# Performance work log

Hardware: AMD Instinct MI355X
Metric: run time of the kernel (lower is better)

## Reference

```python
import jax, jax.numpy as jnp
import numpy as np

N_NODES = 20000
N_EDGES = 320000
NUM_FEATURES = 128
CUTOFF = 5.0
NUM_RBF = 20
EPS = 1e-8


def setup_inputs() -> dict:
    key = jax.random.key(0)
    ks = jax.random.split(key, 10)
    v = jax.random.normal(ks[0], (N_NODES, NUM_FEATURES, 3), dtype=jnp.float32)
    s = jax.random.normal(ks[1], (N_NODES, NUM_FEATURES), dtype=jnp.float32)
    # edge list: col0 = src idx, col1 = dst idx (js), cols 2:5 = displacement vector
    src = jax.random.randint(ks[2], (N_EDGES,), 0, N_NODES).astype(jnp.float32)
    dst = jax.random.randint(ks[3], (N_EDGES,), 0, N_NODES).astype(jnp.float32)
    vec = jax.random.normal(ks[4], (N_EDGES, 3), dtype=jnp.float32) * 2.0
    r = jnp.concatenate([src[:, None], dst[:, None], vec], axis=1)
    # s_path params (torch Linear weight [out,in] -> stored here as [in,out])
    W1 = jax.random.normal(ks[5], (NUM_FEATURES, NUM_FEATURES), dtype=jnp.float32) * np.sqrt(2.0 / NUM_FEATURES)
    b1 = jnp.zeros((NUM_FEATURES,), dtype=jnp.float32)
    W2 = jax.random.normal(ks[6], (NUM_FEATURES, 3 * NUM_FEATURES), dtype=jnp.float32) * np.sqrt(2.0 / NUM_FEATURES)
    b2 = jnp.zeros((3 * NUM_FEATURES,), dtype=jnp.float32)
    # r_path params
    Wr = jax.random.normal(ks[7], (NUM_RBF, 3 * NUM_FEATURES), dtype=jnp.float32) * np.sqrt(1.0 / NUM_RBF)
    br = jnp.zeros((3 * NUM_FEATURES,), dtype=jnp.float32)
    return {"v": v, "s": s, "r": r, "W1": W1, "b1": b1, "W2": W2, "b2": b2, "Wr": Wr, "br": br}


def reference(v, s, r, W1, b1, W2, b2, Wr, br):
    nf = NUM_FEATURES
    js = r[:, 1].astype(jnp.int32)          # [E] destination node indices
    rv = r[:, 2:]                            # [E,3] displacement vectors

    # s_path: Linear -> SiLU -> Linear, computed per-node then gathered
    h = s @ W1 + b1
    phi = (h * jax.nn.sigmoid(h)) @ W2 + b2  # [N, 3*nf]

    # RBF expansion of edge distances
    norm_r = jnp.linalg.norm(rv, axis=1, keepdims=True)          # [E,1]
    norm_c = jnp.clip(norm_r, EPS)
    n = jnp.arange(1, NUM_RBF + 1, dtype=rv.dtype)[None, :]      # [1,20]
    rbf = jnp.clip(jnp.sin(n * (jnp.pi / CUTOFF) * norm_c) / (norm_c + EPS), -1.0, 1.0)

    # r_path Linear then cosine cutoff applied elementwise to the features
    Wf = rbf @ Wr + br                                            # [E, 3*nf]
    Wf = 0.5 * (jnp.cos(jnp.pi * Wf / CUTOFF) + 1.0) * (Wf < CUTOFF).astype(Wf.dtype)

    pre = phi[js, :] * Wf                                         # [E, 3*nf]
    split_1 = pre[:, :nf]
    split_2 = pre[:, nf:2 * nf]
    split_3 = pre[:, 2 * nf:]

    # NOTE: original code divides the normalized vector by the norm again
    rvn = rv / (norm_r + EPS)
    dir_term = rvn / (norm_r + EPS)                               # [E,3]
    left_2 = v[js, :, :] * split_1[:, :, None] + split_3[:, :, None] * dir_term[:, None, :]

    delta_v = jnp.zeros_like(v).at[js].add(left_2)
    delta_s = jnp.zeros_like(s).at[js].add(split_2)
    return (delta_v, delta_s)
```

## Files before the change

kernel.cpp:

```cpp
#include <hip/hip_runtime.h>
#include <math.h>

#define NND 20000
#define NE  320000
#define NF  128
#define NRBF 20
#define DEGCAP 64

typedef float f32x4 __attribute__((ext_vector_type(4)));
typedef short bf16x8 __attribute__((ext_vector_type(8)));

static constexpr float FCUT = 5.0f;
static constexpr float FEPS = 1e-8f;

__device__ __forceinline__ unsigned short f2bf(float x) {
    unsigned int u = __builtin_bit_cast(unsigned int, x);
    u += 0x7FFFu + ((u >> 16) & 1u);
    return (unsigned short)(u >> 16);
}
__device__ __forceinline__ float bf2f(unsigned short h) {
    unsigned int u = ((unsigned int)h) << 16;
    return __builtin_bit_cast(float, u);
}

__global__ __launch_bounds__(256) void scatter2_k(const float* __restrict__ r,
                                                  int* __restrict__ cursor,
                                                  float4* __restrict__ payload) {
    int e = blockIdx.x * 256 + threadIdx.x;
    if (e >= NE) return;
    const float* re = r + (size_t)e * 5;
    int j = (int)re[1];
    float x = re[2], y = re[3], z = re[4];
    float nrm = sqrtf(x * x + y * y + z * z);
    float inv = 1.0f / ((nrm + FEPS) * (nrm + FEPS));
    int pos = atomicAdd(&cursor[j], 1);
    if (pos < DEGCAP)
        payload[((size_t)j << 6) + pos] = make_float4(x * inv, y * inv, z * inv, nrm);
}

__global__ __launch_bounds__(256) void pack_all_k(const float* __restrict__ W1,
                                                  const float* __restrict__ W2,
                                                  const float* __restrict__ Wr,
                                                  const float* __restrict__ br,
                                                  unsigned short* __restrict__ Wp1,
                                                  unsigned short* __restrict__ Wp2,
                                                  unsigned short* __restrict__ WrP) {
    int fid = blockIdx.x * 256 + threadIdx.x;
    if (fid < 2048) {
        int lane = fid & 63, kk = (fid >> 6) & 3, nch = fid >> 8;
        int col = nch * 16 + (lane & 15);
        int k0 = kk * 32 + ((lane >> 4) * 8);
        unsigned short* o = Wp1 + (size_t)fid * 8;
#pragma unroll
        for (int j = 0; j < 8; j++) o[j] = f2bf(W1[(size_t)(k0 + j) * 128 + col]);
    } else if (fid < 2048 + 6144) {
        int f2 = fid - 2048;
        int lane = f2 & 63, kk = (f2 >> 6) & 3, nch = f2 >> 8;
        int col = nch * 16 + (lane & 15);
        int k0 = kk * 32 + ((lane >> 4) * 8);
        unsigned short* o = Wp2 + (size_t)f2 * 8;
#pragma unroll
        for (int j = 0; j < 8; j++) o[j] = f2bf(W2[(size_t)(k0 + j) * 384 + col]);
    } else if (fid < 2048 + 6144 + 1536) {
        int f3 = fid - 8192;
        int lane = f3 & 63, ft = f3 >> 6;
        int col = ft * 16 + (lane & 15);
        int k0 = (lane >> 4) * 8;
        unsigned short* o = WrP + (size_t)f3 * 8;
#pragma unroll
        for (int j = 0; j < 8; j++) {
            int k = k0 + j;
            float val = (k < NRBF) ? Wr[(size_t)k * 384 + col] : ((k == NRBF) ? br[col] : 0.0f);
            o[j] = f2bf(val);
        }
    }
}

__global__ __launch_bounds__(256) void mlp_k(const float* __restrict__ s,
                                             const unsigned short* __restrict__ Wp1,
                                             const float* __restrict__ b1,
                                             const unsigned short* __restrict__ Wp2,
                                             const float* __restrict__ b2,
                                             unsigned short* __restrict__ phi) {
    __shared__ unsigned short lds[4 * 8192];
    int tid = threadIdx.x;
    int lane = tid & 63, wave = tid >> 6;
    int node0 = blockIdx.x * 64 + wave * 16;
    int arow = lane & 15, kgrp = lane >> 4;
    unsigned short* hW = lds + wave * 8192;
    unsigned short* pW = hW + 2048;

    int anode = node0 + arow; if (anode > NND - 1) anode = NND - 1;
    const float* ap = s + (size_t)anode * NF + kgrp * 8;
    bf16x8 afrag[4];
#pragma unroll
    for (int kk = 0; kk < 4; kk++) {
        float4 x0 = *(const float4*)(ap + kk * 32);
        float4 x1 = *(const float4*)(ap + kk * 32 + 4);
        union { unsigned short u[8]; bf16x8 v; } c;
        c.u[0] = f2bf(x0.x); c.u[1] = f2bf(x0.y); c.u[2] = f2bf(x0.z); c.u[3] = f2bf(x0.w);
        c.u[4] = f2bf(x1.x); c.u[5] = f2bf(x1.y); c.u[6] = f2bf(x1.z); c.u[7] = f2bf(x1.w);
        afrag[kk] = c.v;
    }
    f32x4 acc[8];
#pragma unroll
    for (int n = 0; n < 8; n++) acc[n] = (f32x4)(0.0f);
    const bf16x8* W8a = (const bf16x8*)Wp1;
#pragma unroll
    for (int nch = 0; nch < 8; nch++)
#pragma unroll
        for (int kk = 0; kk < 4; kk++)
            acc[nch] = __builtin_amdgcn_mfma_f32_16x16x32_bf16(
                afrag[kk], W8a[(nch * 4 + kk) * 64 + lane], acc[nch], 0, 0, 0);
#pragma unroll
    for (int nch = 0; nch < 8; nch++) {
        int col = nch * 16 + arow;
        float bb = b1[col];
#pragma unroll
        for (int rg = 0; rg < 4; rg++) {
            int row = kgrp * 4 + rg;
            float x = acc[nch][rg] + bb;
            float y = x / (1.0f + __expf(-x));
            hW[row * 128 + col] = f2bf(y);
        }
    }
    __syncthreads();
    bf16x8 hfrag[4];
#pragma unroll
    for (int kk = 0; kk < 4; kk++)
        hfrag[kk] = *(const bf16x8*)(hW + arow * 128 + kk * 32 + kgrp * 8);
#pragma unroll
    for (int c = 0; c < 3; c++) {
        f32x4 acc2[8];
#pragma unroll
        for (int n = 0; n < 8; n++) acc2[n] = (f32x4)(0.0f);
        const bf16x8* W8b = (const bf16x8*)Wp2;
#pragma unroll
        for (int nch = 0; nch < 8; nch++)
#pragma unroll
            for (int kk = 0; kk < 4; kk++)
                acc2[nch] = __builtin_amdgcn_mfma_f32_16x16x32_bf16(
                    hfrag[kk], W8b[((c * 8 + nch) * 4 + kk) * 64 + lane], acc2[nch], 0, 0, 0);
#pragma unroll
        for (int nch = 0; nch < 8; nch++) {
            int colg = c * 128 + nch * 16 + arow;
            float bb = b2[colg];
#pragma unroll
            for (int rg = 0; rg < 4; rg++) {
                int row = kgrp * 4 + rg;
                pW[row * 384 + colg] = f2bf(acc2[nch][rg] + bb);
            }
        }
    }
    __syncthreads();
#pragma unroll
    for (int it = 0; it < 12; it++) {
        int idx = it * 64 + lane;
        int row = idx / 48, ch = idx - row * 48;
        int node = node0 + row;
        if (node < NND) {
            uint4 val = *(const uint4*)(pW + row * 384 + ch * 8);
            *(uint4*)(phi + (size_t)node * 384 + ch * 8) = val;
        }
    }
}

__global__ __launch_bounds__(256) void reduce6_k(const int* __restrict__ cursor,
                                                 const float4* __restrict__ payload,
                                                 const unsigned short* __restrict__ phi,
                                                 const float* __restrict__ v,
                                                 const unsigned short* __restrict__ WrP,
                                                 float* __restrict__ dv,
                                                 float* __restrict__ ds) {
    int tid = threadIdx.x;
    int lane = tid & 63;
    int la = lane & 15, kg = lane >> 4;
    int gwid = blockIdx.x * 4 + (tid >> 6);
    int w = gwid & 1;
    int jstart = gwid >> 1;
    int jstride = (gridDim.x * 4) >> 1;

    bool isKg2 = (kg == 2), isKg3 = (kg == 3);

    bf16x8 wrf[12];
#pragma unroll
    for (int q = 0; q < 12; q++)
        wrf[q] = *(const bf16x8*)(WrP + (size_t)(((2 * q + w) << 6) + lane) * 8);

    for (int j = jstart; j < NND; j += jstride) {
        int deg = cursor[j]; if (deg > DEGCAP) deg = DEGCAP;
        const float4* pay = payload + ((size_t)j << 6);

        int f = (2 * kg + w) * 16 + la;
        const unsigned short* ph = phi + (size_t)j * 384;
        float p1 = bf2f(ph[f]), p2 = bf2f(ph[128 + f]), p3 = bf2f(ph[256 + f]);
        size_t vb = ((size_t)j * NF + f) * 3;
        float vx = v[vb], vy = v[vb + 1], vz = v[vb + 2];

        float a0[4], a1[4], sdx[4], sdy[4], sdz[4];
        float DX = 0.f, DY = 0.f, DZ = 0.f;
#pragma unroll
        for (int i = 0; i < 4; i++) { a0[i] = 0.f; a1[i] = 0.f; sdx[i] = 0.f; sdy[i] = 0.f; sdz[i] = 0.f; }

        for (int base = 0; base < deg; base += 16) {
            int cnt = deg - base; if (cnt > 16) cnt = 16;
            float4 p = pay[base + (la < cnt ? la : cnt - 1)];
            float nc = fmaxf(p.w, FEPS);
            float invd = 1.0f / (nc + FEPS);
            float sv[8];
#pragma unroll
            for (int j2 = 0; j2 < 8; j2++) {
                int k = kg * 8 + j2;
                float s0 = __builtin_amdgcn_sinf((float)(k + 1) * 0.1f * nc) * invd;
                sv[j2] = fminf(fmaxf(s0, -1.f), 1.f);
            }
            unsigned int w0, w1, w2, w3;
            asm("v_cvt_pk_bf16_f32 %0, %1, %2" : "=v"(w0) : "v"(sv[0]), "v"(sv[1]));
            asm("v_cvt_pk_bf16_f32 %0, %1, %2" : "=v"(w1) : "v"(sv[2]), "v"(sv[3]));
            asm("v_cvt_pk_bf16_f32 %0, %1, %2" : "=v"(w2) : "v"(sv[4]), "v"(sv[5]));
            asm("v_cvt_pk_bf16_f32 %0, %1, %2" : "=v"(w3) : "v"(sv[6]), "v"(sv[7]));
            w2 = isKg2 ? 0x00003F80u : w2;
            w0 = isKg3 ? 0u : w0;
            w1 = isKg3 ? 0u : w1;
            w2 = isKg3 ? 0u : w2;
            w3 = (kg >= 2) ? 0u : w3;
            union { unsigned int w[4]; bf16x8 v8; } af;
            af.w[0] = w0; af.w[1] = w1; af.w[2] = w2; af.w[3] = w3;
            float dx[4], dy[4], dz[4], lim[4];
#pragma unroll
            for (int rr = 0; rr < 4; rr++) {
                int er = kg * 4 + rr;
                dx[rr] = __shfl(p.x, er);
                dy[rr] = __shfl(p.y, er);
                dz[rr] = __shfl(p.z, er);
                lim[rr] = (er < cnt) ? FCUT : -3.4e38f;
            }
            DX += dx[0] + dx[1] + dx[2] + dx[3];
            DY += dy[0] + dy[1] + dy[2] + dy[3];
            DZ += dz[0] + dz[1] + dz[2] + dz[3];
#pragma unroll
            for (int q = 0; q < 12; q++) {
                f32x4 d = __builtin_amdgcn_mfma_f32_16x16x32_bf16(
                    af.v8, wrf[q], (f32x4)(0.0f), 0, 0, 0);
#pragma unroll
                for (int rr = 0; rr < 4; rr++) {
                    float a = d[rr];
                    float c = __builtin_amdgcn_cosf(a * 0.1f);
                    float t = (a < lim[rr]) ? c : -1.0f;
                    if (q < 4)      a0[q] += t;
                    else if (q < 8) a1[q - 4] += t;
                    else {
                        sdx[q - 8] = fmaf(t, dx[rr], sdx[q - 8]);
                        sdy[q - 8] = fmaf(t, dy[rr], sdy[q - 8]);
                        sdz[q - 8] = fmaf(t, dz[rr], sdz[q - 8]);
                    }
                }
            }
        }
#pragma unroll
        for (int i = 0; i < 4; i++) {
            a0[i] += __shfl_xor(a0[i], 16);  a0[i] += __shfl_xor(a0[i], 32);
            a1[i] += __shfl_xor(a1[i], 16);  a1[i] += __shfl_xor(a1[i], 32);
            sdx[i] += __shfl_xor(sdx[i], 16); sdx[i] += __shfl_xor(sdx[i], 32);
            sdy[i] += __shfl_xor(sdy[i], 16); sdy[i] += __shfl_xor(sdy[i], 32);
            sdz[i] += __shfl_xor(sdz[i], 16); sdz[i] += __shfl_xor(sdz[i], 32);
        }
        DX += __shfl_xor(DX, 16); DX += __shfl_xor(DX, 32);
        DY += __shfl_xor(DY, 16); DY += __shfl_xor(DY, 32);
        DZ += __shfl_xor(DZ, 16); DZ += __shfl_xor(DZ, 32);
        float R = (float)(((deg + 15) >> 4) << 4);

        float A0 = 0, A1 = 0, SX = 0, SY = 0, SZ = 0;
#pragma unroll
        for (int i = 0; i < 4; i++) {
            if (kg == i) { A0 = a0[i]; A1 = a1[i]; SX = sdx[i]; SY = sdy[i]; SZ = sdz[i]; }
        }
        float sum1 = 0.5f * (A0 + R);
        float sum2 = 0.5f * (A1 + R);
        float sx = 0.5f * (SX + DX);
        float sy = 0.5f * (SY + DY);
        float sz = 0.5f * (SZ + DZ);

        ds[(size_t)j * NF + f] = p2 * sum2;
        float c1 = p1 * sum1;
        dv[vb + 0] = fmaf(vx, c1, p3 * sx);
        dv[vb + 1] = fmaf(vy, c1, p3 * sy);
        dv[vb + 2] = fmaf(vz, c1, p3 * sz);
    }
}

extern "C" void kernel_launch(void* const* d_in, const int* in_sizes, int n_in,
                              void* d_out, int out_size, void* d_ws, size_t ws_size,
                              hipStream_t stream) {
    const float* v  = (const float*)d_in[0];
    const float* s  = (const float*)d_in[1];
    const float* r  = (const float*)d_in[2];
    const float* W1 = (const float*)d_in[3];
    const float* b1 = (const float*)d_in[4];
    const float* W2 = (const float*)d_in[5];
    const float* b2 = (const float*)d_in[6];
    const float* Wr = (const float*)d_in[7];
    const float* br = (const float*)d_in[8];

    float* dv = (float*)d_out;
    float* ds = dv + (size_t)NND * NF * 3;

    char* ws = (char*)d_ws;
    int* cursor             = (int*)ws;
    float* payload          = (float*)(ws + 80128);
    unsigned short* Wp1     = (unsigned short*)(ws + 20560128);
    unsigned short* Wp2     = (unsigned short*)(ws + 20592896);
    unsigned short* WrP     = (unsigned short*)(ws + 20691200);
    unsigned short* phi     = (unsigned short*)(ws + 20715776);

    hipMemsetAsync(cursor, 0, NND * sizeof(int), stream);
    scatter2_k<<<(NE + 255) / 256, 256, 0, stream>>>(r, cursor, (float4*)payload);

    pack_all_k<<<38, 256, 0, stream>>>(W1, W2, Wr, br, Wp1, Wp2, WrP);

    mlp_k<<<(NND + 63) / 64, 256, 0, stream>>>(s, Wp1, b1, Wp2, b2, phi);

    reduce6_k<<<2560, 256, 0, stream>>>(cursor, (const float4*)payload, phi, v, WrP, dv, ds);
}
```

Measured before the change: 114.9 us.

## Fold cutoff mask and scale into RBF weights, prefetch payload, merge prep kernels

Wr and br are pre-scaled by 0.1 when packed, and an extra bf16 weight row of 1.0 is added. Padded edge rows get a large value in that slot, so after the MFMA a single fminf clamp gives the cutoff and padding mask inside the cosine argument. This replaces the per-element multiply, compare and select in the reduce inner loop. The next tile's payload is now loaded one iteration ahead, and the edge scatter and weight-packing kernels are merged into a single launch. The cost is extra code paths, and bf16 rounding now applies to the 0.1-scaled weights.

```diff
diff --git a/kernel.cpp b/kernel.cpp
--- a/kernel.cpp
+++ b/kernel.cpp
@@ -6,6 +6,7 @@
 #define NF  128
 #define NRBF 20
 #define DEGCAP 64
+#define SCATB 1250
 
 typedef float f32x4 __attribute__((ext_vector_type(4)));
 typedef short bf16x8 __attribute__((ext_vector_type(8)));
@@ -23,29 +24,30 @@
     return __builtin_bit_cast(float, u);
 }
 
-__global__ __launch_bounds__(256) void scatter2_k(const float* __restrict__ r,
-                                                  int* __restrict__ cursor,
-                                                  float4* __restrict__ payload) {
-    int e = blockIdx.x * 256 + threadIdx.x;
-    if (e >= NE) return;
-    const float* re = r + (size_t)e * 5;
-    int j = (int)re[1];
-    float x = re[2], y = re[3], z = re[4];
-    float nrm = sqrtf(x * x + y * y + z * z);
-    float inv = 1.0f / ((nrm + FEPS) * (nrm + FEPS));
-    int pos = atomicAdd(&cursor[j], 1);
-    if (pos < DEGCAP)
-        payload[((size_t)j << 6) + pos] = make_float4(x * inv, y * inv, z * inv, nrm);
-}
-
-__global__ __launch_bounds__(256) void pack_all_k(const float* __restrict__ W1,
-                                                  const float* __restrict__ W2,
-                                                  const float* __restrict__ Wr,
-                                                  const float* __restrict__ br,
-                                                  unsigned short* __restrict__ Wp1,
-                                                  unsigned short* __restrict__ Wp2,
-                                                  unsigned short* __restrict__ WrP) {
-    int fid = blockIdx.x * 256 + threadIdx.x;
+__global__ __launch_bounds__(256) void prep_k(const float* __restrict__ r,
+                                              int* __restrict__ cursor,
+                                              float4* __restrict__ payload,
+                                              const float* __restrict__ W1,
+                                              const float* __restrict__ W2,
+                                              const float* __restrict__ Wr,
+                                              const float* __restrict__ br,
+                                              unsigned short* __restrict__ Wp1,
+                                              unsigned short* __restrict__ Wp2,
+                                              unsigned short* __restrict__ WrP) {
+    if (blockIdx.x < SCATB) {
+        int e = blockIdx.x * 256 + threadIdx.x;
+        if (e >= NE) return;
+        const float* re = r + (size_t)e * 5;
+        int j = (int)re[1];
+        float x = re[2], y = re[3], z = re[4];
+        float nrm = sqrtf(x * x + y * y + z * z);
+        float inv = 1.0f / ((nrm + FEPS) * (nrm + FEPS));
+        int pos = atomicAdd(&cursor[j], 1);
+        if (pos < DEGCAP)
+            payload[((size_t)j << 6) + pos] = make_float4(x * inv, y * inv, z * inv, nrm);
+        return;
+    }
+    int fid = (blockIdx.x - SCATB) * 256 + threadIdx.x;
     if (fid < 2048) {
         int lane = fid & 63, kk = (fid >> 6) & 3, nch = fid >> 8;
         int col = nch * 16 + (lane & 15);
@@ -70,7 +72,11 @@
 #pragma unroll
         for (int j = 0; j < 8; j++) {
             int k = k0 + j;
-            float val = (k < NRBF) ? Wr[(size_t)k * 384 + col] : ((k == NRBF) ? br[col] : 0.0f);
+            float val;
+            if (k < NRBF)            val = 0.1f * Wr[(size_t)k * 384 + col];
+            else if (k == NRBF)      val = 0.1f * br[col];
+            else if (k == NRBF + 1)  val = 1.0f;
+            else                     val = 0.0f;
             o[j] = f2bf(val);
         }
     }
@@ -165,7 +171,7 @@
     }
 }
 
-__global__ __launch_bounds__(256) void reduce6_k(const int* __restrict__ cursor,
+__global__ __launch_bounds__(256) void reduce7_k(const int* __restrict__ cursor,
                                                  const float4* __restrict__ payload,
                                                  const unsigned short* __restrict__ phi,
                                                  const float* __restrict__ v,
@@ -202,9 +208,18 @@
 #pragma unroll
         for (int i = 0; i < 4; i++) { a0[i] = 0.f; a1[i] = 0.f; sdx[i] = 0.f; sdy[i] = 0.f; sdz[i] = 0.f; }
 
-        for (int base = 0; base < deg; base += 16) {
-            int cnt = deg - base; if (cnt > 16) cnt = 16;
-            float4 p = pay[base + (la < cnt ? la : cnt - 1)];
+        int ntiles = (deg + 15) >> 4;
+        float4 p_next;
+        if (deg > 0) p_next = pay[la < deg ? la : deg - 1];
+
+        for (int t5 = 0; t5 < ntiles; t5++) {
+            float4 p = p_next;
+            if (t5 + 1 < ntiles) {
+                int idx = (t5 + 1) * 16 + la;
+                p_next = pay[idx < deg ? idx : deg - 1];
+            }
+            int cnt = deg - t5 * 16; if (cnt > 16) cnt = 16;
+
             float nc = fmaxf(p.w, FEPS);
             float invd = 1.0f / (nc + FEPS);
             float sv[8];
@@ -219,34 +234,33 @@
             asm("v_cvt_pk_bf16_f32 %0, %1, %2" : "=v"(w1) : "v"(sv[2]), "v"(sv[3]));
             asm("v_cvt_pk_bf16_f32 %0, %1, %2" : "=v"(w2) : "v"(sv[4]), "v"(sv[5]));
             asm("v_cvt_pk_bf16_f32 %0, %1, %2" : "=v"(w3) : "v"(sv[6]), "v"(sv[7]));
-            w2 = isKg2 ? 0x00003F80u : w2;
+            w2 = isKg2 ? ((la < cnt) ? 0x00003F80u : 0x41203F80u) : w2;
             w0 = isKg3 ? 0u : w0;
             w1 = isKg3 ? 0u : w1;
             w2 = isKg3 ? 0u : w2;
             w3 = (kg >= 2) ? 0u : w3;
-            union { unsigned int w[4]; bf16x8 v8; } af;
-            af.w[0] = w0; af.w[1] = w1; af.w[2] = w2; af.w[3] = w3;
-            float dx[4], dy[4], dz[4], lim[4];
+            union { unsigned int wrd[4]; bf16x8 v8; } af;
+            af.wrd[0] = w0; af.wrd[1] = w1; af.wrd[2] = w2; af.wrd[3] = w3;
+
+            float dx[4], dy[4], dz[4];
 #pragma unroll
             for (int rr = 0; rr < 4; rr++) {
                 int er = kg * 4 + rr;
                 dx[rr] = __shfl(p.x, er);
                 dy[rr] = __shfl(p.y, er);
                 dz[rr] = __shfl(p.z, er);
-                lim[rr] = (er < cnt) ? FCUT : -3.4e38f;
             }
             DX += dx[0] + dx[1] + dx[2] + dx[3];
             DY += dy[0] + dy[1] + dy[2] + dy[3];
             DZ += dz[0] + dz[1] + dz[2] + dz[3];
+
 #pragma unroll
             for (int q = 0; q < 12; q++) {
                 f32x4 d = __builtin_amdgcn_mfma_f32_16x16x32_bf16(
                     af.v8, wrf[q], (f32x4)(0.0f), 0, 0, 0);
 #pragma unroll
                 for (int rr = 0; rr < 4; rr++) {
-                    float a = d[rr];
-                    float c = __builtin_amdgcn_cosf(a * 0.1f);
-                    float t = (a < lim[rr]) ? c : -1.0f;
+                    float t = __builtin_amdgcn_cosf(fminf(d[rr], 0.5f));
                     if (q < 4)      a0[q] += t;
                     else if (q < 8) a1[q - 4] += t;
                     else {
@@ -314,11 +328,10 @@
     unsigned short* phi     = (unsigned short*)(ws + 20715776);
 
     hipMemsetAsync(cursor, 0, NND * sizeof(int), stream);
-    scatter2_k<<<(NE + 255) / 256, 256, 0, stream>>>(r, cursor, (float4*)payload);
-
-    pack_all_k<<<38, 256, 0, stream>>>(W1, W2, Wr, br, Wp1, Wp2, WrP);
+    prep_k<<<SCATB + 38, 256, 0, stream>>>(r, cursor, (float4*)payload,
+                                           W1, W2, Wr, br, Wp1, Wp2, WrP);
 
     mlp_k<<<(NND + 63) / 64, 256, 0, stream>>>(s, Wp1, b1, Wp2, b2, phi);
 
-    reduce6_k<<<2560, 256, 0, stream>>>(cursor, (const float4*)payload, phi, v, WrP, dv, ds);
-}
+    reduce7_k<<<2560, 256, 0, stream>>>(cursor, (const float4*)payload, phi, v, WrP, dv, ds);
+}
```

Result: faster. 109.7 us (-4.5%).
